# Optimization experiments

Measured on AMD Instinct MI355X. Metric: run time of the kernel, lower is better.

The kernel has to match this reference:

```python
import jax, jax.numpy as jnp
import numpy as np

B, N, H, L, R, E = 8, 10000, 64, 4, 3, 200000
FP, NUM_CELLS = 2048, 100
LN_EPS = 1e-3  # Keras LayerNormalization default epsilon


def setup_inputs() -> dict:
    key = jax.random.key(0)
    ks = jax.random.split(key, 24)
    g = lambda k, shape, fan: (jax.random.uniform(k, shape, jnp.float32) * 2 - 1) * np.sqrt(6.0 / fan)
    inp = {
        'ctl_expr': jax.random.normal(ks[0], (B, N), jnp.float32),
        'drug_targets': jax.random.uniform(ks[1], (B, N), jnp.float32),
        'drug_fp': jax.random.uniform(ks[2], (B, FP), jnp.float32),
        'edge_weight': jax.random.uniform(ks[3], (R, E), jnp.float32),
        'cell_idx': jax.random.randint(ks[4], (B,), 0, NUM_CELLS, jnp.int32),
        'edge_index': jax.random.randint(ks[5], (R, 2, E), 0, N, jnp.int32),
        # parameters
        'W_se': g(ks[6], (1, H), 1 + H),
        'b_se': jnp.zeros((H,), jnp.float32),
        'cell_emb': jax.random.normal(ks[7], (NUM_CELLS, H), jnp.float32) * 0.05,
        'W_f1': g(ks[8], (FP, H), FP + H),
        'b_f1': jnp.zeros((H,), jnp.float32),
        'W_f2': g(ks[9], (H, 2 * H), 3 * H) * 0.1,
        'b_f2': jnp.zeros((2 * H,), jnp.float32),
        'Wself': jnp.stack([g(ks[10 + l], (H, H), 2 * H) for l in range(L)]),
        'Wrel': jnp.stack([jnp.stack([g(jax.random.fold_in(ks[14], l * R + r), (H, H), 2 * H) for r in range(R)]) for l in range(L)]),
        'ln_g': jnp.ones((L, H), jnp.float32),
        'ln_b': jnp.zeros((L, H), jnp.float32),
        'W_out': g(ks[15], (H, 1), H + 1),
        'b_out': jnp.zeros((1,), jnp.float32),
    }
    return inp


def reference(ctl_expr, drug_targets, drug_fp, edge_weight, cell_idx, edge_index,
              W_se, b_se, cell_emb, W_f1, b_f1, W_f2, b_f2,
              Wself, Wrel, ln_g, ln_b, W_out, b_out):
    # shared_embedding: Dense(H, relu) applied to scalar node features
    def shared(v):  # v: [B,N] -> [B,N,H]
        return jax.nn.relu(v[..., None] * W_se[0] + b_se)

    x = shared(ctl_expr) + shared(drug_targets)            # [B,N,H]
    x = x + cell_emb[cell_idx][:, None, :]                 # cell embedding broadcast

    # drug FiLM: gamma/beta conditioning
    film = jax.nn.relu(drug_fp @ W_f1 + b_f1) @ W_f2 + b_f2  # [B,2H]
    gamma, beta = jnp.split(film, 2, axis=-1)
    gamma = jnp.tanh(gamma)
    x = x * (1.0 + gamma[:, None, :]) + beta[:, None, :]

    n_layers, n_rel = Wself.shape[0], Wrel.shape[1]
    for l in range(n_layers):
        out = x @ Wself[l]                                 # self projection [B,N,H]
        for r in range(n_rel):
            src, dst = edge_index[r, 0], edge_index[r, 1]
            h = x @ Wrel[l, r]                             # [B,N,H]
            msg = edge_weight[r][None, :, None] * h[:, src, :]  # [B,E,H]
            out = out.at[:, dst].add(msg)                  # scatter-add to dst nodes
        # LayerNorm over feature dim (Keras eps=1e-3)
        mu = out.mean(-1, keepdims=True)
        var = ((out - mu) ** 2).mean(-1, keepdims=True)
        out = (out - mu) * jax.lax.rsqrt(var + LN_EPS) * ln_g[l] + ln_b[l]
        x = jax.nn.relu(out)

    return (x @ W_out)[..., 0] + b_out[0]                  # [B,N]
```

## Files before the change

kernel.cpp:

```cpp
#include <hip/hip_runtime.h>
#include <hip/hip_bf16.h>
#include <math.h>

#define Bk 8
#define Nk 10000
#define Hk 64
#define Lk 4
#define Rk 3
#define Ek 200000
#define FPk 2048

#define C4 (Rk*Ek/4)
#define CNT4B ((C4 + 255)/256)
#define INITB 2048
#define DEGW  (Rk*Nk*16)

typedef unsigned short u16;
typedef unsigned int   u32;
typedef _Float16 f16;
typedef __attribute__((ext_vector_type(2))) _Float16 f16x2;
typedef __attribute__((ext_vector_type(8))) _Float16 f16x8;
typedef __attribute__((ext_vector_type(4))) float f32x4;

__device__ __forceinline__ f16x2 as_h2(u32 u){
    union{u32 i; f16x2 h;} v; v.i = u; return v.h;
}
__device__ __forceinline__ u16 f2h_bits(float f){
    union{f16 h; u16 u;} v; v.h = (f16)f; return v.u;
}

__global__ void k_prep0(const float* __restrict__ Wself, const float* __restrict__ Wrel,
                        u16* __restrict__ wt, int* __restrict__ deg,
                        const float* __restrict__ fp, const float* __restrict__ W1,
                        const float* __restrict__ b1, float* __restrict__ hid){
    __shared__ float red[256];
    if(blockIdx.x < 256){
        int idx = blockIdx.x*256 + threadIdx.x;
        if(idx < DEGW/8){
            *(int4*)&deg[idx*8]     = make_int4(0,0,0,0);
            *(int4*)&deg[idx*8 + 4] = make_int4(0,0,0,0);
        }
        int j    = idx & 7;
        int lane = (idx >> 3) & 63;
        int jt   = (idx >> 9) & 3;
        int kc   = (idx >> 11) & 1;
        int mt   = (idx >> 12) & 3;
        int l    = idx >> 14;
        int k    = kc*32 + (lane >> 4)*8 + j;
        int col  = jt*16 + (lane & 15);
        float w = (mt == 0) ? Wself[(l*64 + k)*64 + col]
                            : Wrel[((l*3 + (mt-1))*64 + k)*64 + col];
        wt[idx] = f2h_bits(w);
    }else{
        int bb = blockIdx.x - 256;
        int b = bb >> 6, h = bb & 63;
        const float* fpb = fp + b*FPk;
        float acc = 0.f;
        for(int k = threadIdx.x; k < FPk; k += 256)
            acc += fpb[k] * W1[k*64 + h];
        red[threadIdx.x] = acc;
        __syncthreads();
        for(int s = 128; s >= 1; s >>= 1){
            if(threadIdx.x < s) red[threadIdx.x] += red[threadIdx.x + s];
            __syncthreads();
        }
        if(threadIdx.x == 0) hid[b*64 + h] = fmaxf(red[0] + b1[h], 0.f);
    }
}

__global__ void k_efill(const int* __restrict__ edge_index, const float* __restrict__ edge_weight,
                        int* __restrict__ deg, u32* __restrict__ epack){
    int idx = blockIdx.x*256 + threadIdx.x;
    if(idx >= C4) return;
    int g = idx*4;
    int r = g / Ek, e = g % Ek;
    int4   s4 = *(const int4*)  &edge_index [r*2*Ek + e];
    int4   d4 = *(const int4*)  &edge_index [r*2*Ek + Ek + e];
    float4 w4 = *(const float4*)&edge_weight[r*Ek + e];
    int* dg = deg + (size_t)r*Nk*16;
    size_t ebase = (size_t)r*Nk;
    int pos;
    pos = atomicAdd(&dg[(size_t)d4.x*16], 1);
    if(pos < 64) epack[((ebase + d4.x) << 6) + pos] = ((u32)f2h_bits(w4.x) << 16) | (u32)s4.x;
    pos = atomicAdd(&dg[(size_t)d4.y*16], 1);
    if(pos < 64) epack[((ebase + d4.y) << 6) + pos] = ((u32)f2h_bits(w4.y) << 16) | (u32)s4.y;
    pos = atomicAdd(&dg[(size_t)d4.z*16], 1);
    if(pos < 64) epack[((ebase + d4.z) << 6) + pos] = ((u32)f2h_bits(w4.z) << 16) | (u32)s4.z;
    pos = atomicAdd(&dg[(size_t)d4.w*16], 1);
    if(pos < 64) epack[((ebase + d4.w) << 6) + pos] = ((u32)f2h_bits(w4.w) << 16) | (u32)s4.w;
}

__global__ void k_xinit(const float* __restrict__ ctl, const float* __restrict__ dt,
                        const int* __restrict__ cell_idx,
                        const float* __restrict__ W_se, const float* __restrict__ b_se,
                        const float* __restrict__ cell_emb,
                        const float* __restrict__ hid, const float* __restrict__ W2,
                        const float* __restrict__ b2,
                        u16* __restrict__ xh){
    __shared__ float g1l[64], btl[64];
    int b   = blockIdx.x >> 8;
    int blk = blockIdx.x & 255;
    int t = threadIdx.x;
    if(t < 128){
        float acc = b2[t];
        #pragma unroll 8
        for(int k = 0; k < 64; ++k)
            acc += hid[b*64 + k] * W2[k*128 + t];
        if(t < 64) g1l[t] = 1.f + tanhf(acc);
        else       btl[t - 64] = acc;
    }
    __syncthreads();
    int ci = cell_idx[b];
    const int per_b = Nk*8;
    for(int o = blk*256 + t; o < per_b; o += 256*256){
        int hq = o & 7;
        int n  = o >> 3;
        float c = ctl[b*Nk + n], d = dt[b*Nk + n];
        u32 pk[4];
        #pragma unroll
        for(int j = 0; j < 8; j += 2){
            int h0 = hq*8 + j, h1 = h0 + 1;
            float w0 = W_se[h0], s0 = b_se[h0];
            float w1 = W_se[h1], s1 = b_se[h1];
            float v0 = fmaxf(c*w0 + s0, 0.f) + fmaxf(d*w0 + s0, 0.f)
                     + cell_emb[ci*64 + h0];
            float v1 = fmaxf(c*w1 + s1, 0.f) + fmaxf(d*w1 + s1, 0.f)
                     + cell_emb[ci*64 + h1];
            v0 = v0 * g1l[h0] + btl[h0];
            v1 = v1 * g1l[h1] + btl[h1];
            pk[j >> 1] = (u32)f2h_bits(v0) | ((u32)f2h_bits(v1) << 16);
        }
        *(int4*)&xh[(((size_t)b*Nk + n)*64) + hq*8] = make_int4(pk[0], pk[1], pk[2], pk[3]);
    }
}

__global__ __launch_bounds__(256) void k_agg(const u16* __restrict__ xh,
                      const int* __restrict__ deg, const u32* __restrict__ epack,
                      u16* __restrict__ aggh){
    __shared__ int2 stash[4][64];
    int bpair = blockIdx.x & 3;
    int grp   = blockIdx.x >> 2;
    int wq    = threadIdx.x >> 6;
    int wid   = grp*4 + wq;
    int lane  = threadIdx.x & 63;
    int fg    = lane & 31;
    int bl    = lane >> 5;
    int b     = bpair*2 + bl;
    int r = wid / Nk, dst = wid % Nk;
    int cnt = deg[(size_t)wid*16]; if(cnt > 64) cnt = 64;
    const u32* ep = epack + ((size_t)wid << 6);
    const char* xb = (const char*)xh + (size_t)b*Nk*128 + fg*4;

    f16x2 A = (f16x2){0,0}, C = (f16x2){0,0};
    int2* st = stash[wq];
    if(lane < cnt){
        u32 e = ep[lane];
        st[lane] = make_int2((int)((e & 0xFFFFu) << 7),
                             (int)((e >> 16) | (e & 0xFFFF0000u)));
    }
    int t = 0;
    for(; t + 8 <= cnt; t += 8){
        int4 q01 = *(const int4*)&st[t];
        int4 q23 = *(const int4*)&st[t+2];
        int4 q45 = *(const int4*)&st[t+4];
        int4 q67 = *(const int4*)&st[t+6];
        u32 u0 = *(const u32*)(xb + q01.x);
        u32 u1 = *(const u32*)(xb + q01.z);
        u32 u2 = *(const u32*)(xb + q23.x);
        u32 u3 = *(const u32*)(xb + q23.z);
        u32 u4 = *(const u32*)(xb + q45.x);
        u32 u5 = *(const u32*)(xb + q45.z);
        u32 u6 = *(const u32*)(xb + q67.x);
        u32 u7 = *(const u32*)(xb + q67.z);
        A += as_h2(u0)*as_h2(q01.y); C += as_h2(u1)*as_h2(q01.w);
        A += as_h2(u2)*as_h2(q23.y); C += as_h2(u3)*as_h2(q23.w);
        A += as_h2(u4)*as_h2(q45.y); C += as_h2(u5)*as_h2(q45.w);
        A += as_h2(u6)*as_h2(q67.y); C += as_h2(u7)*as_h2(q67.w);
    }
    for(; t + 2 <= cnt; t += 2){
        int4 q01 = *(const int4*)&st[t];
        u32 u0 = *(const u32*)(xb + q01.x);
        u32 u1 = *(const u32*)(xb + q01.z);
        A += as_h2(u0)*as_h2(q01.y); C += as_h2(u1)*as_h2(q01.w);
    }
    if(t < cnt){
        int2 p = st[t];
        u32 u = *(const u32*)(xb + p.x);
        A += as_h2(u)*as_h2(p.y);
    }
    float a0 = (float)A.x + (float)C.x;
    float a1 = (float)A.y + (float)C.y;
    u32 packed = (u32)f2h_bits(a0) | ((u32)f2h_bits(a1) << 16);
    ((u32*)aggh)[(((size_t)r*Bk + b)*Nk + dst)*32 + fg] = packed;
}

__global__ __launch_bounds__(256) void k_proj_mfma(u16* __restrict__ xh,
        const u16* __restrict__ aggh, const u16* __restrict__ wt,
        const float* __restrict__ ln_g, const float* __restrict__ ln_b, int l,
        int last, const float* __restrict__ W_out, const float* __restrict__ b_out,
        float* __restrict__ out){
    __shared__ u16 wls[16384];
    const u16* wl = wt + (size_t)l*16384;
    for(int i = threadIdx.x; i < 2048; i += 256)
        *(int4*)&wls[i*8] = *(const int4*)&wl[i*8];
    __syncthreads();

    int lane = threadIdx.x & 63;
    int wq   = threadIdx.x >> 6;
    int k8   = blockIdx.x & 7;
    int b    = ((k8 & 3) << 1) | (k8 >> 2);
    int tile = blockIdx.x >> 3;
    int n0   = tile*64 + wq*16;
    int mrow = lane & 15;
    int kq   = lane >> 4;
    int nA = n0 + mrow; if(nA >= Nk) nA = Nk - 1;

    f32x4 acc[4];
    #pragma unroll
    for(int jt = 0; jt < 4; ++jt) acc[jt] = (f32x4){0.f,0.f,0.f,0.f};

    #pragma unroll
    for(int mt = 0; mt < 4; ++mt){
        const u16* arowA = ((mt == 0)
            ? xh   + (size_t)b*Nk*64
            : aggh + (((size_t)(mt-1)*Bk + b)*Nk)*64) + (size_t)nA*64;
        #pragma unroll
        for(int kc = 0; kc < 2; ++kc){
            f16x8 aA = *(const f16x8*)(arowA + kc*32 + kq*8);
            #pragma unroll
            for(int jt = 0; jt < 4; ++jt){
                f16x8 bfrag = *(const f16x8*)(wls + ((size_t)((mt*2 + kc)*4 + jt)*64 + lane)*8);
                acc[jt] = __builtin_amdgcn_mfma_f32_16x16x32_f16(aA, bfrag, acc[jt], 0, 0, 0);
            }
        }
    }

    float gv[4], bv[4], wo[4];
    #pragma unroll
    for(int jt = 0; jt < 4; ++jt){
        int f = jt*16 + mrow;
        gv[jt] = ln_g[l*64 + f];
        bv[jt] = ln_b[l*64 + f];
        wo[jt] = W_out[f];
    }
    float bo = b_out[0];
    u16* xdst = xh + (size_t)b*Nk*64;

    #pragma unroll
    for(int v = 0; v < 4; ++v){
        float s1 = acc[0][v] + acc[1][v] + acc[2][v] + acc[3][v];
        float s2 = acc[0][v]*acc[0][v] + acc[1][v]*acc[1][v]
                 + acc[2][v]*acc[2][v] + acc[3][v]*acc[3][v];
        #pragma unroll
        for(int off = 1; off <= 8; off <<= 1){
            s1 += __shfl_xor(s1, off);
            s2 += __shfl_xor(s2, off);
        }
        float mu  = s1 * 0.015625f;
        float var = s2 * 0.015625f - mu*mu;
        float rstd = rsqrtf(var + 1e-3f);
        int node = n0 + kq*4 + v;
        if(!last){
            if(node < Nk){
                #pragma unroll
                for(int jt = 0; jt < 4; ++jt){
                    float o = (acc[jt][v] - mu) * rstd * gv[jt] + bv[jt];
                    xdst[(size_t)node*64 + jt*16 + mrow] = f2h_bits(fmaxf(o, 0.f));
                }
            }
        }else{
            float s3 = 0.f;
            #pragma unroll
            for(int jt = 0; jt < 4; ++jt){
                float o = (acc[jt][v] - mu) * rstd * gv[jt] + bv[jt];
                s3 += fmaxf(o, 0.f) * wo[jt];
            }
            #pragma unroll
            for(int off = 1; off <= 8; off <<= 1)
                s3 += __shfl_xor(s3, off);
            if(mrow == 0 && node < Nk)
                out[(size_t)b*Nk + node] = s3 + bo;
        }
    }
}

extern "C" void kernel_launch(void* const* d_in, const int* in_sizes, int n_in,
                              void* d_out, int out_size, void* d_ws, size_t ws_size,
                              hipStream_t stream){
    const float* ctl        = (const float*)d_in[0];
    const float* dt         = (const float*)d_in[1];
    const float* drug_fp    = (const float*)d_in[2];
    const float* edge_w     = (const float*)d_in[3];
    const int*   cell_idx   = (const int*)  d_in[4];
    const int*   edge_index = (const int*)  d_in[5];
    const float* W_se       = (const float*)d_in[6];
    const float* b_se       = (const float*)d_in[7];
    const float* cell_emb   = (const float*)d_in[8];
    const float* W_f1       = (const float*)d_in[9];
    const float* b_f1       = (const float*)d_in[10];
    const float* W_f2       = (const float*)d_in[11];
    const float* b_f2       = (const float*)d_in[12];
    const float* Wself      = (const float*)d_in[13];
    const float* Wrel       = (const float*)d_in[14];
    const float* ln_g       = (const float*)d_in[15];
    const float* ln_b       = (const float*)d_in[16];
    const float* W_out      = (const float*)d_in[17];
    const float* b_out      = (const float*)d_in[18];
    float* out = (float*)d_out;

    char* p = (char*)d_ws;
    auto alloc = [&](size_t bytes)->char*{
        char* r = p; p += (bytes + 255) & ~(size_t)255; return r;
    };
    int*   deg    = (int*)  alloc((size_t)DEGW*4);
    u32*   epack  = (u32*)  alloc((size_t)Rk*Nk*64*4);
    float* hid    = (float*)alloc((size_t)Bk*64*4);
    u16*   xh     = (u16*)  alloc((size_t)Bk*Nk*64*2);
    u16*   aggh   = (u16*)  alloc((size_t)3*Bk*Nk*64*2);
    u16*   wt     = (u16*)  alloc((size_t)Lk*16384*2);

    k_prep0<<<256 + Bk*64, 256, 0, stream>>>(Wself, Wrel, wt, deg,
                                             drug_fp, W_f1, b_f1, hid);
    k_efill<<<CNT4B, 256, 0, stream>>>(edge_index, edge_w, deg, epack);
    k_xinit<<<INITB, 256, 0, stream>>>(ctl, dt, cell_idx, W_se, b_se, cell_emb,
                                       hid, W_f2, b_f2, xh);

    const int ntile = (Nk + 63)/64;
    for(int l = 0; l < Lk; ++l){
        k_agg<<<4*7500, 256, 0, stream>>>(xh, deg, epack, aggh);
        k_proj_mfma<<<ntile*8, 256, 0, stream>>>(
            xh, aggh, wt, ln_g, ln_b, l,
            (l == Lk-1) ? 1 : 0, W_out, b_out, out);
    }
}
```

Before: 362.5 us.

## Merge edge fill and x init into one launch, partition edge fill by dst range

Combines the edge-bucketing kernel and the node-feature init kernel into a single launch so they can run concurrently. The edge fill is split into 8 destination-range partitions, each block pass handling only edges whose dst falls in its range. The aim is to localize atomic counters and epack writes per partition and overlap the two independent kernels. The cost is reading the dst indices eight times. Partitioning also changes the order in which slots are assigned within a bucket, which can change which edges survive the 64-cap and the summation order.

```diff
diff --git a/kernel.cpp b/kernel.cpp
--- a/kernel.cpp
+++ b/kernel.cpp
@@ -11,9 +11,10 @@
 #define FPk 2048
 
 #define C4 (Rk*Ek/4)
-#define CNT4B ((C4 + 255)/256)
+#define EFB ((C4 + 255)/256)
 #define INITB 2048
 #define DEGW  (Rk*Nk*16)
+#define NPART 1250
 
 typedef unsigned short u16;
 typedef unsigned int   u32;
@@ -68,69 +69,83 @@
     }
 }
 
-__global__ void k_efill(const int* __restrict__ edge_index, const float* __restrict__ edge_weight,
-                        int* __restrict__ deg, u32* __restrict__ epack){
-    int idx = blockIdx.x*256 + threadIdx.x;
-    if(idx >= C4) return;
-    int g = idx*4;
-    int r = g / Ek, e = g % Ek;
-    int4   s4 = *(const int4*)  &edge_index [r*2*Ek + e];
-    int4   d4 = *(const int4*)  &edge_index [r*2*Ek + Ek + e];
-    float4 w4 = *(const float4*)&edge_weight[r*Ek + e];
-    int* dg = deg + (size_t)r*Nk*16;
-    size_t ebase = (size_t)r*Nk;
-    int pos;
-    pos = atomicAdd(&dg[(size_t)d4.x*16], 1);
-    if(pos < 64) epack[((ebase + d4.x) << 6) + pos] = ((u32)f2h_bits(w4.x) << 16) | (u32)s4.x;
-    pos = atomicAdd(&dg[(size_t)d4.y*16], 1);
-    if(pos < 64) epack[((ebase + d4.y) << 6) + pos] = ((u32)f2h_bits(w4.y) << 16) | (u32)s4.y;
-    pos = atomicAdd(&dg[(size_t)d4.z*16], 1);
-    if(pos < 64) epack[((ebase + d4.z) << 6) + pos] = ((u32)f2h_bits(w4.z) << 16) | (u32)s4.z;
-    pos = atomicAdd(&dg[(size_t)d4.w*16], 1);
-    if(pos < 64) epack[((ebase + d4.w) << 6) + pos] = ((u32)f2h_bits(w4.w) << 16) | (u32)s4.w;
-}
-
-__global__ void k_xinit(const float* __restrict__ ctl, const float* __restrict__ dt,
-                        const int* __restrict__ cell_idx,
-                        const float* __restrict__ W_se, const float* __restrict__ b_se,
-                        const float* __restrict__ cell_emb,
-                        const float* __restrict__ hid, const float* __restrict__ W2,
-                        const float* __restrict__ b2,
-                        u16* __restrict__ xh){
+__global__ void k_efx(const int* __restrict__ edge_index, const float* __restrict__ edge_weight,
+                      int* __restrict__ deg, u32* __restrict__ epack,
+                      const float* __restrict__ ctl, const float* __restrict__ dt,
+                      const int* __restrict__ cell_idx,
+                      const float* __restrict__ W_se, const float* __restrict__ b_se,
+                      const float* __restrict__ cell_emb,
+                      const float* __restrict__ hid, const float* __restrict__ W2,
+                      const float* __restrict__ b2,
+                      u16* __restrict__ xh){
     __shared__ float g1l[64], btl[64];
-    int b   = blockIdx.x >> 8;
-    int blk = blockIdx.x & 255;
-    int t = threadIdx.x;
-    if(t < 128){
-        float acc = b2[t];
-        #pragma unroll 8
-        for(int k = 0; k < 64; ++k)
-            acc += hid[b*64 + k] * W2[k*128 + t];
-        if(t < 64) g1l[t] = 1.f + tanhf(acc);
-        else       btl[t - 64] = acc;
-    }
-    __syncthreads();
-    int ci = cell_idx[b];
-    const int per_b = Nk*8;
-    for(int o = blk*256 + t; o < per_b; o += 256*256){
-        int hq = o & 7;
-        int n  = o >> 3;
-        float c = ctl[b*Nk + n], d = dt[b*Nk + n];
-        u32 pk[4];
-        #pragma unroll
-        for(int j = 0; j < 8; j += 2){
-            int h0 = hq*8 + j, h1 = h0 + 1;
-            float w0 = W_se[h0], s0 = b_se[h0];
-            float w1 = W_se[h1], s1 = b_se[h1];
-            float v0 = fmaxf(c*w0 + s0, 0.f) + fmaxf(d*w0 + s0, 0.f)
-                     + cell_emb[ci*64 + h0];
-            float v1 = fmaxf(c*w1 + s1, 0.f) + fmaxf(d*w1 + s1, 0.f)
-                     + cell_emb[ci*64 + h1];
-            v0 = v0 * g1l[h0] + btl[h0];
-            v1 = v1 * g1l[h1] + btl[h1];
-            pk[j >> 1] = (u32)f2h_bits(v0) | ((u32)f2h_bits(v1) << 16);
-        }
-        *(int4*)&xh[(((size_t)b*Nk + n)*64) + hq*8] = make_int4(pk[0], pk[1], pk[2], pk[3]);
+    if(blockIdx.x < 8*EFB){
+        int part = blockIdx.x & 7;
+        int idx  = (blockIdx.x >> 3)*256 + threadIdx.x;
+        if(idx >= C4) return;
+        int g = idx*4;
+        int r = g / Ek, e = g % Ek;
+        int4   d4 = *(const int4*)  &edge_index [r*2*Ek + Ek + e];
+        int lo = part*NPART, hi = lo + NPART;
+        if((d4.x < lo || d4.x >= hi) && (d4.y < lo || d4.y >= hi) &&
+           (d4.z < lo || d4.z >= hi) && (d4.w < lo || d4.w >= hi)) return;
+        int4   s4 = *(const int4*)  &edge_index [r*2*Ek + e];
+        float4 w4 = *(const float4*)&edge_weight[r*Ek + e];
+        int* dg = deg + (size_t)r*Nk*16;
+        size_t ebase = (size_t)r*Nk;
+        int pos;
+        if(d4.x >= lo && d4.x < hi){
+            pos = atomicAdd(&dg[(size_t)d4.x*16], 1);
+            if(pos < 64) epack[((ebase + d4.x) << 6) + pos] = ((u32)f2h_bits(w4.x) << 16) | (u32)s4.x;
+        }
+        if(d4.y >= lo && d4.y < hi){
+            pos = atomicAdd(&dg[(size_t)d4.y*16], 1);
+            if(pos < 64) epack[((ebase + d4.y) << 6) + pos] = ((u32)f2h_bits(w4.y) << 16) | (u32)s4.y;
+        }
+        if(d4.z >= lo && d4.z < hi){
+            pos = atomicAdd(&dg[(size_t)d4.z*16], 1);
+            if(pos < 64) epack[((ebase + d4.z) << 6) + pos] = ((u32)f2h_bits(w4.z) << 16) | (u32)s4.z;
+        }
+        if(d4.w >= lo && d4.w < hi){
+            pos = atomicAdd(&dg[(size_t)d4.w*16], 1);
+            if(pos < 64) epack[((ebase + d4.w) << 6) + pos] = ((u32)f2h_bits(w4.w) << 16) | (u32)s4.w;
+        }
+    }else{
+        int vb  = blockIdx.x - 8*EFB;
+        int b   = vb >> 8;
+        int blk = vb & 255;
+        int t = threadIdx.x;
+        if(t < 128){
+            float acc = b2[t];
+            #pragma unroll 8
+            for(int k = 0; k < 64; ++k)
+                acc += hid[b*64 + k] * W2[k*128 + t];
+            if(t < 64) g1l[t] = 1.f + tanhf(acc);
+            else       btl[t - 64] = acc;
+        }
+        __syncthreads();
+        int ci = cell_idx[b];
+        const int per_b = Nk*8;
+        for(int o = blk*256 + t; o < per_b; o += 256*256){
+            int hq = o & 7;
+            int n  = o >> 3;
+            float c = ctl[b*Nk + n], d = dt[b*Nk + n];
+            u32 pk[4];
+            #pragma unroll
+            for(int j = 0; j < 8; j += 2){
+                int h0 = hq*8 + j, h1 = h0 + 1;
+                float w0 = W_se[h0], s0 = b_se[h0];
+                float w1 = W_se[h1], s1 = b_se[h1];
+                float v0 = fmaxf(c*w0 + s0, 0.f) + fmaxf(d*w0 + s0, 0.f)
+                         + cell_emb[ci*64 + h0];
+                float v1 = fmaxf(c*w1 + s1, 0.f) + fmaxf(d*w1 + s1, 0.f)
+                         + cell_emb[ci*64 + h1];
+                v0 = v0 * g1l[h0] + btl[h0];
+                v1 = v1 * g1l[h1] + btl[h1];
+                pk[j >> 1] = (u32)f2h_bits(v0) | ((u32)f2h_bits(v1) << 16);
+            }
+            *(int4*)&xh[(((size_t)b*Nk + n)*64) + hq*8] = make_int4(pk[0], pk[1], pk[2], pk[3]);
+        }
     }
 }
 
@@ -321,9 +336,9 @@
 
     k_prep0<<<256 + Bk*64, 256, 0, stream>>>(Wself, Wrel, wt, deg,
                                              drug_fp, W_f1, b_f1, hid);
-    k_efill<<<CNT4B, 256, 0, stream>>>(edge_index, edge_w, deg, epack);
-    k_xinit<<<INITB, 256, 0, stream>>>(ctl, dt, cell_idx, W_se, b_se, cell_emb,
-                                       hid, W_f2, b_f2, xh);
+    k_efx<<<8*EFB + INITB, 256, 0, stream>>>(edge_index, edge_w, deg, epack,
+                                             ctl, dt, cell_idx, W_se, b_se, cell_emb,
+                                             hid, W_f2, b_f2, xh);
 
     const int ntile = (Nk + 63)/64;
     for(int l = 0; l < Lk; ++l){
```

Result: no change. 356.1 us (-1.8%).
